# Kernel optimization log

Measured on AMD Instinct MI355X. Metric: run time of the kernel, lower is better.

## Reference

```python
import jax, jax.numpy as jnp
import numpy as np

B = 64
C = 12        # num_classes
NC = 16       # num_clusters
N0, N1, N2, N3, NDIM = 2048, 1000, 500, 100, 3
E = C * NC    # 192 residual heads


def _init(key, shape, fan_in):
    return jax.random.normal(key, shape, dtype=jnp.float32) / np.sqrt(fan_in)


def setup_inputs() -> dict:
    key = jax.random.key(0)
    ks = jax.random.split(key, 12)
    x = jax.random.normal(ks[0], (B, N0), dtype=jnp.float32)
    class_label = jax.random.randint(ks[1], (B, 1), 0, C)
    return {
        'x': x,
        'class_label': class_label,
        # bin_3layer weights, stacked over the class axis
        'W1b': _init(ks[2], (C, N1, N0), N0),
        'b1b': jnp.zeros((C, N1), jnp.float32),
        'W2b': _init(ks[3], (C, N2, N1), N1),
        'b2b': jnp.zeros((C, N2), jnp.float32),
        'W3b': _init(ks[4], (C, NC, N2), N2),
        'b3b': jnp.zeros((C, NC), jnp.float32),
        # res_2layer weights, stacked over class*cluster axis
        'W1r': _init(ks[5], (E, N3, N0), N0),
        'b1r': jnp.zeros((E, N3), jnp.float32),
        'W2r': _init(ks[6], (E, NDIM, N3), N3),
        'b2r': jnp.zeros((E, NDIM), jnp.float32),
    }


def reference(x, class_label, W1b, b1b, W2b, b2b, W3b, b3b, W1r, b1r, W2r, b2r):
    # --- bin heads: all classes computed (as the torch loop does), grouped GEMMs ---
    h = jax.nn.relu(jnp.einsum('bi,cji->bcj', x, W1b) + b1b)        # [B,C,N1]
    h = jax.nn.relu(jnp.einsum('bcj,ckj->bck', h, W2b) + b2b)       # [B,C,N2]
    y1_all = jnp.einsum('bck,cmk->bcm', h, W3b) + b3b               # [B,C,NC]

    # --- res heads: all class*cluster experts computed ---
    r = jax.nn.relu(jnp.einsum('bi,eji->bej', x, W1r) + b1r)        # [B,E,N3]
    y2_all = jnp.einsum('bej,edj->bed', r, W2r) + b2r               # [B,E,NDIM]
    y2_all = y2_all.reshape(B, C, NC, NDIM)

    # one-hot bmm over class axis == gather per-sample class
    cl = class_label[:, 0]                                           # [B]
    y1 = jnp.take_along_axis(y1_all, cl[:, None, None], axis=1)[:, 0]        # [B,NC]
    y2c = jnp.take_along_axis(y2_all, cl[:, None, None, None], axis=1)[:, 0] # [B,NC,NDIM]

    # argmax over clusters, then one-hot bmm over cluster axis == gather
    pose = jnp.argmax(y1, axis=1)                                    # [B]
    y2 = jnp.take_along_axis(y2c, pose[:, None, None], axis=1)[:, 0] # [B,NDIM]
    return y1, y2
```

## Files before the change

### kernel.cpp

```cpp
#include <hip/hip_runtime.h>

#define B_   64
#define C_   12
#define NC_  16
#define N0_  2048
#define N1_  1000
#define N2_  500
#define N3_  100
#define AGENT __HIP_MEMORY_SCOPE_AGENT

__device__ __forceinline__ float wred(float v) {
#pragma unroll
    for (int off = 32; off > 0; off >>= 1) v += __shfl_xor(v, off, 64);
    return v;
}

__global__ __launch_bounds__(256)
void k_l1b(const float* __restrict__ x, const int* __restrict__ cls,
           const float* __restrict__ W1b, const float* __restrict__ b1b,
           float* __restrict__ h1, int* __restrict__ zbase) {
    if (blockIdx.x == 0 && blockIdx.y == 0) {
        for (int i = threadIdx.x; i < 1408; i += 256) zbase[i] = 0;
    }
    const int c    = blockIdx.y;
    const int lane = threadIdx.x & 63;
    const int wave = threadIdx.x >> 6;
    const unsigned long long m = __ballot(cls[lane] == c);
    if (m == 0ull) return;

    const int j0 = blockIdx.x * 16 + wave * 4;
    if (j0 >= N1_) return;

    const float* wbase = W1b + ((size_t)c * N1_ + j0) * N0_;
    float4 w[4][8];
#pragma unroll
    for (int k = 0; k < 4; ++k) {
        const float4* wr = (const float4*)(wbase + (size_t)k * N0_);
#pragma unroll
        for (int f = 0; f < 8; ++f) w[k][f] = wr[f * 64 + lane];
    }
    const float4 bias = *(const float4*)(b1b + c * N1_ + j0);

    for (unsigned long long mm = m; mm; mm &= (mm - 1ull)) {
        const int b = (int)__builtin_ctzll(mm);
        const float4* xr = (const float4*)(x + (size_t)b * N0_);
        float a0 = 0.f, a1 = 0.f, a2 = 0.f, a3 = 0.f;
#pragma unroll
        for (int f = 0; f < 8; ++f) {
            const float4 xv = xr[f * 64 + lane];
            a0 += w[0][f].x * xv.x + w[0][f].y * xv.y + w[0][f].z * xv.z + w[0][f].w * xv.w;
            a1 += w[1][f].x * xv.x + w[1][f].y * xv.y + w[1][f].z * xv.z + w[1][f].w * xv.w;
            a2 += w[2][f].x * xv.x + w[2][f].y * xv.y + w[2][f].z * xv.z + w[2][f].w * xv.w;
            a3 += w[3][f].x * xv.x + w[3][f].y * xv.y + w[3][f].z * xv.z + w[3][f].w * xv.w;
        }
        const float s0 = wred(a0), s1 = wred(a1), s2 = wred(a2), s3 = wred(a3);
        if (lane == 0) {
            float4 hv;
            hv.x = fmaxf(s0 + bias.x, 0.f);
            hv.y = fmaxf(s1 + bias.y, 0.f);
            hv.z = fmaxf(s2 + bias.z, 0.f);
            hv.w = fmaxf(s3 + bias.w, 0.f);
            *(float4*)(h1 + (size_t)b * N1_ + j0) = hv;
        }
    }
}

__global__ __launch_bounds__(1024)
void k_perb(const float* __restrict__ x, const int* __restrict__ cls,
            const float* __restrict__ h1,
            const float* __restrict__ W2b, const float* __restrict__ b2b,
            const float* __restrict__ W3b, const float* __restrict__ b3b,
            const float* __restrict__ W1r, const float* __restrict__ b1r,
            const float* __restrict__ W2r, const float* __restrict__ b2r,
            float* __restrict__ y1acc, int* __restrict__ cntb,
            int* __restrict__ flag,  int* __restrict__ cnt2,
            float* __restrict__ y2acc,
            float* __restrict__ out_y1, float* __restrict__ out_y2) {
    const int b    = blockIdx.x >> 2;
    const int q    = blockIdx.x & 3;
    const int tid  = threadIdx.x;
    const int lane = tid & 63;
    const int wave = tid >> 6;
    const int c    = cls[b];

    __shared__ __align__(16) float s_x[N0_];
    __shared__ __align__(16) float s_h1[N1_];
    __shared__ float s_part[16][16];
    __shared__ int   s_e;

    {
        const float4* xs = (const float4*)(x  + (size_t)b * N0_);
        const float4* hs = (const float4*)(h1 + (size_t)b * N1_);
        float4* xd = (float4*)s_x;
        float4* hd = (float4*)s_h1;
        if (tid < 512) xd[tid] = xs[tid];
        else if (tid < 512 + 250) hd[tid - 512] = hs[tid - 512];
    }
    __syncthreads();

    float accm = 0.f;
    for (int idx = wave; idx < 125; idx += 16) {
        const int j = 4 * idx + q;
        const float4* wr = (const float4*)(W2b + ((size_t)c * N2_ + j) * N1_);
        const float4* xr = (const float4*)s_h1;
        float a = 0.f;
#pragma unroll
        for (int f = 0; f < 4; ++f) {
            const int id4 = f * 64 + lane;
            if (id4 < N1_ / 4) {
                const float4 wv = wr[id4], xv = xr[id4];
                a += wv.x * xv.x + wv.y * xv.y + wv.z * xv.z + wv.w * xv.w;
            }
        }
        const float h2v = fmaxf(wred(a) + b2b[c * N2_ + j], 0.f);
        if (lane < NC_) accm += h2v * W3b[((size_t)c * NC_ + lane) * N2_ + j];
    }
    if (lane < NC_) s_part[wave][lane] = accm;
    __syncthreads();

    if (wave == 0) {
        if (lane < NC_) {
            float t = 0.f;
#pragma unroll
            for (int w = 0; w < 16; ++w) t += s_part[w][lane];
            __hip_atomic_fetch_add(&y1acc[b * NC_ + lane], t, __ATOMIC_RELAXED, AGENT);
        }
        int old = 0;
        if (lane == 0) old = __hip_atomic_fetch_add(&cntb[b], 1, __ATOMIC_ACQ_REL, AGENT);
        old = __shfl(old, 0, 64);
        if (old == 3) {
            float v = -1e30f;
            if (lane < NC_) {
                v = __hip_atomic_load(&y1acc[b * NC_ + lane], __ATOMIC_RELAXED, AGENT)
                    + b3b[c * NC_ + lane];
                out_y1[b * NC_ + lane] = v;
            }
            int mi = lane;
#pragma unroll
            for (int off = 8; off > 0; off >>= 1) {
                const float ov = __shfl_xor(v,  off, 16);
                const int   om = __shfl_xor(mi, off, 16);
                if (ov > v || (ov == v && om < mi)) { v = ov; mi = om; }
            }
            if (lane == 0)
                __hip_atomic_store(&flag[b], 1 + c * NC_ + mi, __ATOMIC_RELEASE, AGENT);
        }
        int fv = 0;
        if (lane == 0) {
            while ((fv = __hip_atomic_load(&flag[b], __ATOMIC_RELAXED, AGENT)) == 0)
                __builtin_amdgcn_s_sleep(1);
            s_e = fv - 1;
        }
    }
    __syncthreads();
    const int e = s_e;

    float y2p = 0.f;
    for (int idx = wave; idx < 25; idx += 16) {
        const int j = 4 * idx + q;
        const float4* wr = (const float4*)(W1r + ((size_t)e * N3_ + j) * N0_);
        const float4* xr = (const float4*)s_x;
        float a = 0.f;
#pragma unroll
        for (int f = 0; f < 8; ++f) {
            const int id4 = f * 64 + lane;
            const float4 wv = wr[id4], xv = xr[id4];
            a += wv.x * xv.x + wv.y * xv.y + wv.z * xv.z + wv.w * xv.w;
        }
        const float rv = fmaxf(wred(a) + b1r[e * N3_ + j], 0.f);
        if (lane < 3) y2p += rv * W2r[((size_t)e * 3 + lane) * N3_ + j];
    }
    if (lane < NC_) s_part[wave][lane] = (lane < 3) ? y2p : 0.f;
    __syncthreads();

    if (wave == 0) {
        if (lane < 3) {
            float t = 0.f;
#pragma unroll
            for (int w = 0; w < 16; ++w) t += s_part[w][lane];
            __hip_atomic_fetch_add(&y2acc[b * 3 + lane], t, __ATOMIC_RELAXED, AGENT);
        }
        int old = 0;
        if (lane == 0) old = __hip_atomic_fetch_add(&cnt2[b], 1, __ATOMIC_ACQ_REL, AGENT);
        old = __shfl(old, 0, 64);
        if (old == 3 && lane < 3) {
            const float vv = __hip_atomic_load(&y2acc[b * 3 + lane], __ATOMIC_RELAXED, AGENT);
            out_y2[b * 3 + lane] = vv + b2r[e * 3 + lane];
        }
    }
}

extern "C" void kernel_launch(void* const* d_in, const int* in_sizes, int n_in,
                              void* d_out, int out_size, void* d_ws, size_t ws_size,
                              hipStream_t stream) {
    const float* x   = (const float*)d_in[0];
    const int*   cls = (const int*)  d_in[1];
    const float* W1b = (const float*)d_in[2];
    const float* b1b = (const float*)d_in[3];
    const float* W2b = (const float*)d_in[4];
    const float* b2b = (const float*)d_in[5];
    const float* W3b = (const float*)d_in[6];
    const float* b3b = (const float*)d_in[7];
    const float* W1r = (const float*)d_in[8];
    const float* b1r = (const float*)d_in[9];
    const float* W2r = (const float*)d_in[10];
    const float* b2r = (const float*)d_in[11];

    float* out_y1 = (float*)d_out;
    float* out_y2 = (float*)d_out + B_ * NC_;

    char*  ws    = (char*)d_ws;
    float* h1    = (float*)(ws);
    float* y1acc = (float*)(ws + 256000);
    int*   cntb  = (int*)  (ws + 260096);
    int*   flag  = (int*)  (ws + 260352);
    int*   cnt2  = (int*)  (ws + 260608);
    float* y2acc = (float*)(ws + 260864);
    int*   zbase = (int*)  (ws + 256000);

    hipLaunchKernelGGL(k_l1b, dim3(63, 12), dim3(256), 0, stream,
                       x, cls, W1b, b1b, h1, zbase);
    hipLaunchKernelGGL(k_perb, dim3(256), dim3(1024), 0, stream,
                       x, cls, h1, W2b, b2b, W3b, b3b, W1r, b1r, W2r, b2r,
                       y1acc, cntb, flag, cnt2, y2acc, out_y1, out_y2);
}
```

Before: 73.12 us.

## Halve rows per wave in layer-1, stage W3 in LDS, replace float atomics with partials

The first kernel now gives each wave 2 output rows instead of 4 and doubles the grid to 125x12 blocks. This exposes more parallel waves for streaming the W1b weights and lowers register pressure. The second kernel preloads the class's W3 slice into shared memory so the per-row loop no longer does strided global loads. It also replaces float atomic accumulation with per-quarter partial buffers that the last-arriving block sums, adding thread fences and a smaller zeroing region.

```diff
diff --git a/kernel.cpp b/kernel.cpp
--- a/kernel.cpp
+++ b/kernel.cpp
@@ -20,7 +20,7 @@
            const float* __restrict__ W1b, const float* __restrict__ b1b,
            float* __restrict__ h1, int* __restrict__ zbase) {
     if (blockIdx.x == 0 && blockIdx.y == 0) {
-        for (int i = threadIdx.x; i < 1408; i += 256) zbase[i] = 0;
+        if (threadIdx.x < 192) zbase[threadIdx.x] = 0;
     }
     const int c    = blockIdx.y;
     const int lane = threadIdx.x & 63;
@@ -28,39 +28,29 @@
     const unsigned long long m = __ballot(cls[lane] == c);
     if (m == 0ull) return;
 
-    const int j0 = blockIdx.x * 16 + wave * 4;
-    if (j0 >= N1_) return;
-
-    const float* wbase = W1b + ((size_t)c * N1_ + j0) * N0_;
-    float4 w[4][8];
-#pragma unroll
-    for (int k = 0; k < 4; ++k) {
-        const float4* wr = (const float4*)(wbase + (size_t)k * N0_);
-#pragma unroll
-        for (int f = 0; f < 8; ++f) w[k][f] = wr[f * 64 + lane];
-    }
-    const float4 bias = *(const float4*)(b1b + c * N1_ + j0);
+    const int j0 = blockIdx.x * 8 + wave * 2;
+    const float4* wr0 = (const float4*)(W1b + ((size_t)c * N1_ + j0) * N0_);
+    const float4* wr1 = wr0 + (N0_ / 4);
+    float4 w0[8], w1[8];
+#pragma unroll
+    for (int f = 0; f < 8; ++f) { w0[f] = wr0[f * 64 + lane]; w1[f] = wr1[f * 64 + lane]; }
+    const float bias0 = b1b[c * N1_ + j0];
+    const float bias1 = b1b[c * N1_ + j0 + 1];
 
     for (unsigned long long mm = m; mm; mm &= (mm - 1ull)) {
         const int b = (int)__builtin_ctzll(mm);
         const float4* xr = (const float4*)(x + (size_t)b * N0_);
-        float a0 = 0.f, a1 = 0.f, a2 = 0.f, a3 = 0.f;
+        float a0 = 0.f, a1 = 0.f;
 #pragma unroll
         for (int f = 0; f < 8; ++f) {
             const float4 xv = xr[f * 64 + lane];
-            a0 += w[0][f].x * xv.x + w[0][f].y * xv.y + w[0][f].z * xv.z + w[0][f].w * xv.w;
-            a1 += w[1][f].x * xv.x + w[1][f].y * xv.y + w[1][f].z * xv.z + w[1][f].w * xv.w;
-            a2 += w[2][f].x * xv.x + w[2][f].y * xv.y + w[2][f].z * xv.z + w[2][f].w * xv.w;
-            a3 += w[3][f].x * xv.x + w[3][f].y * xv.y + w[3][f].z * xv.z + w[3][f].w * xv.w;
-        }
-        const float s0 = wred(a0), s1 = wred(a1), s2 = wred(a2), s3 = wred(a3);
+            a0 += w0[f].x * xv.x + w0[f].y * xv.y + w0[f].z * xv.z + w0[f].w * xv.w;
+            a1 += w1[f].x * xv.x + w1[f].y * xv.y + w1[f].z * xv.z + w1[f].w * xv.w;
+        }
+        const float s0 = wred(a0), s1 = wred(a1);
         if (lane == 0) {
-            float4 hv;
-            hv.x = fmaxf(s0 + bias.x, 0.f);
-            hv.y = fmaxf(s1 + bias.y, 0.f);
-            hv.z = fmaxf(s2 + bias.z, 0.f);
-            hv.w = fmaxf(s3 + bias.w, 0.f);
-            *(float4*)(h1 + (size_t)b * N1_ + j0) = hv;
+            h1[(size_t)b * N1_ + j0]     = fmaxf(s0 + bias0, 0.f);
+            h1[(size_t)b * N1_ + j0 + 1] = fmaxf(s1 + bias1, 0.f);
         }
     }
 }
@@ -72,9 +62,8 @@
             const float* __restrict__ W3b, const float* __restrict__ b3b,
             const float* __restrict__ W1r, const float* __restrict__ b1r,
             const float* __restrict__ W2r, const float* __restrict__ b2r,
-            float* __restrict__ y1acc, int* __restrict__ cntb,
-            int* __restrict__ flag,  int* __restrict__ cnt2,
-            float* __restrict__ y2acc,
+            float* __restrict__ y1part, float* __restrict__ y2part,
+            int* __restrict__ cntb, int* __restrict__ cnt2, int* __restrict__ flag,
             float* __restrict__ out_y1, float* __restrict__ out_y2) {
     const int b    = blockIdx.x >> 2;
     const int q    = blockIdx.x & 3;
@@ -85,16 +74,19 @@
 
     __shared__ __align__(16) float s_x[N0_];
     __shared__ __align__(16) float s_h1[N1_];
+    __shared__ float s_w3[NC_][125];
     __shared__ float s_part[16][16];
     __shared__ int   s_e;
 
     {
         const float4* xs = (const float4*)(x  + (size_t)b * N0_);
         const float4* hs = (const float4*)(h1 + (size_t)b * N1_);
-        float4* xd = (float4*)s_x;
-        float4* hd = (float4*)s_h1;
-        if (tid < 512) xd[tid] = xs[tid];
-        else if (tid < 512 + 250) hd[tid - 512] = hs[tid - 512];
+        if (tid < 512) ((float4*)s_x)[tid] = xs[tid];
+        else if (tid < 512 + 250) ((float4*)s_h1)[tid - 512] = hs[tid - 512];
+    }
+    for (int i = tid; i < NC_ * 125; i += 1024) {
+        const int mi = i / 125, idx = i - mi * 125;
+        s_w3[mi][idx] = W3b[((size_t)c * NC_ + mi) * N2_ + 4 * idx + q];
     }
     __syncthreads();
 
@@ -113,7 +105,7 @@
             }
         }
         const float h2v = fmaxf(wred(a) + b2b[c * N2_ + j], 0.f);
-        if (lane < NC_) accm += h2v * W3b[((size_t)c * NC_ + lane) * N2_ + j];
+        if (lane < NC_) accm += h2v * s_w3[lane][idx];
     }
     if (lane < NC_) s_part[wave][lane] = accm;
     __syncthreads();
@@ -123,16 +115,18 @@
             float t = 0.f;
 #pragma unroll
             for (int w = 0; w < 16; ++w) t += s_part[w][lane];
-            __hip_atomic_fetch_add(&y1acc[b * NC_ + lane], t, __ATOMIC_RELAXED, AGENT);
-        }
+            y1part[(size_t)(b * 4 + q) * NC_ + lane] = t;
+        }
+        __threadfence();
         int old = 0;
         if (lane == 0) old = __hip_atomic_fetch_add(&cntb[b], 1, __ATOMIC_ACQ_REL, AGENT);
         old = __shfl(old, 0, 64);
         if (old == 3) {
             float v = -1e30f;
             if (lane < NC_) {
-                v = __hip_atomic_load(&y1acc[b * NC_ + lane], __ATOMIC_RELAXED, AGENT)
-                    + b3b[c * NC_ + lane];
+                v = b3b[c * NC_ + lane];
+#pragma unroll
+                for (int qq = 0; qq < 4; ++qq) v += y1part[(size_t)(b * 4 + qq) * NC_ + lane];
                 out_y1[b * NC_ + lane] = v;
             }
             int mi = lane;
@@ -178,14 +172,17 @@
             float t = 0.f;
 #pragma unroll
             for (int w = 0; w < 16; ++w) t += s_part[w][lane];
-            __hip_atomic_fetch_add(&y2acc[b * 3 + lane], t, __ATOMIC_RELAXED, AGENT);
-        }
+            y2part[(size_t)(b * 4 + q) * 3 + lane] = t;
+        }
+        __threadfence();
         int old = 0;
         if (lane == 0) old = __hip_atomic_fetch_add(&cnt2[b], 1, __ATOMIC_ACQ_REL, AGENT);
         old = __shfl(old, 0, 64);
         if (old == 3 && lane < 3) {
-            const float vv = __hip_atomic_load(&y2acc[b * 3 + lane], __ATOMIC_RELAXED, AGENT);
-            out_y2[b * 3 + lane] = vv + b2r[e * 3 + lane];
+            float t = b2r[e * 3 + lane];
+#pragma unroll
+            for (int qq = 0; qq < 4; ++qq) t += y2part[(size_t)(b * 4 + qq) * 3 + lane];
+            out_y2[b * 3 + lane] = t;
         }
     }
 }
@@ -209,18 +206,18 @@
     float* out_y1 = (float*)d_out;
     float* out_y2 = (float*)d_out + B_ * NC_;
 
-    char*  ws    = (char*)d_ws;
-    float* h1    = (float*)(ws);
-    float* y1acc = (float*)(ws + 256000);
-    int*   cntb  = (int*)  (ws + 260096);
-    int*   flag  = (int*)  (ws + 260352);
-    int*   cnt2  = (int*)  (ws + 260608);
-    float* y2acc = (float*)(ws + 260864);
-    int*   zbase = (int*)  (ws + 256000);
-
-    hipLaunchKernelGGL(k_l1b, dim3(63, 12), dim3(256), 0, stream,
+    char*  ws     = (char*)d_ws;
+    float* h1     = (float*)(ws);
+    float* y1part = (float*)(ws + 256000);
+    float* y2part = (float*)(ws + 272384);
+    int*   cntb   = (int*)  (ws + 275456);
+    int*   cnt2   = (int*)  (ws + 275712);
+    int*   flag   = (int*)  (ws + 275968);
+    int*   zbase  = (int*)  (ws + 275456);
+
+    hipLaunchKernelGGL(k_l1b, dim3(125, 12), dim3(256), 0, stream,
                        x, cls, W1b, b1b, h1, zbase);
     hipLaunchKernelGGL(k_perb, dim3(256), dim3(1024), 0, stream,
                        x, cls, h1, W2b, b2b, W3b, b3b, W1r, b1r, W2r, b2r,
-                       y1acc, cntb, flag, cnt2, y2acc, out_y1, out_y2);
-}
+                       y1part, y2part, cntb, cnt2, flag, out_y1, out_y2);
+}
```

After: 69.83 us. 1.05x faster.
